# Performance work log

Measured on AMD Instinct MI355X. Metric: run time of the kernel, lower is better.

## Reference

```python
import jax, jax.numpy as jnp
import numpy as np

EPS = 1e-6
CHUNK = 64
GATE_LOGIT_NORMALIZER = 16.0
NUM_HEADS = 4


def _rms(x, w):
    return x * jax.lax.rsqrt(jnp.mean(x * x, axis=-1, keepdims=True) + EPS) * w


def _gla_chunk(q, k, v, glog, num_heads):
    # q,k: [B,T,Dk] v: [B,T,Dv] glog: [B,T,Dk] (log decay, <=0)
    B, T, Dk = q.shape
    Dv = v.shape[-1]
    dk, dv = Dk // num_heads, Dv // num_heads
    Nc = T // CHUNK

    def split(x, d):
        # [B,T,H*d] -> [B,H,Nc,C,d]
        return x.reshape(B, T, num_heads, d).transpose(0, 2, 1, 3).reshape(B, num_heads, Nc, CHUNK, d)

    q, k, v, g = split(q, dk), split(k, dk), split(v, dv), split(glog, dk)
    b = jnp.cumsum(g, axis=3)  # inclusive cumulative log-decay within chunk
    scale = dk ** -0.5
    qe = q * jnp.exp(b) * scale

    # intra-chunk: A[t,s] = sum_d q_t k_s exp(b_t - b_s), causal (t>=s)
    mask = jnp.tril(jnp.ones((CHUNK, CHUNK), dtype=bool))
    A = jnp.einsum('bhncd,bhnsd->bhncs', qe, k * jnp.exp(-b))
    A = jnp.where(mask, A, 0.0)
    o_intra = jnp.einsum('bhncs,bhnsd->bhncd', A, v)

    # inter-chunk recurrence over state S: [B,H,dk,dv]
    def step(S, xs):
        qe_c, k_c, v_c, b_c = xs  # [B,H,C,*]
        blast = b_c[:, :, -1, :]                      # [B,H,dk]
        o_inter = jnp.einsum('bhcd,bhde->bhce', qe_c, S)
        kd = k_c * jnp.exp(blast[:, :, None, :] - b_c)
        S_new = S * jnp.exp(blast)[..., None] + jnp.einsum('bhcd,bhce->bhde', kd, v_c)
        return S_new, o_inter

    S0 = jnp.zeros((B, num_heads, dk, dv), q.dtype)
    xs = tuple(jnp.moveaxis(t, 2, 0) for t in (qe, k, v, b))
    _, o_inter = jax.lax.scan(step, S0, xs)
    o = o_intra + jnp.moveaxis(o_inter, 0, 2)  # [B,H,Nc,C,dv]
    return o.reshape(B, num_heads, T, dv).transpose(0, 2, 1, 3)  # [B,T,H,dv]


def setup_inputs() -> dict:
    key = jax.random.key(0)
    ks = jax.random.split(key, 12)
    B, T, Hs = 4, 2048, 1024
    Dk, Dv, I, R = 512, 1024, 2816, 16
    p = lambda k, s: jax.random.normal(k, s, jnp.float32) * 0.02
    return {
        'hidden_states': jax.random.normal(ks[0], (B, T, Hs), jnp.float32),
        'attn_norm_w': jnp.ones((Hs,), jnp.float32),
        'Wq': p(ks[1], (Hs, Dk)), 'Wk': p(ks[2], (Hs, Dk)), 'Wv': p(ks[3], (Hs, Dv)),
        'Wg': p(ks[4], (Hs, Dv)),
        'Wgk1': p(ks[5], (Hs, R)), 'Wgk2': p(ks[6], (R, Dk)), 'bgk2': jnp.zeros((Dk,), jnp.float32),
        'gnorm_w': jnp.ones((Dv // NUM_HEADS,), jnp.float32),
        'Wo': p(ks[7], (Dv, Hs)),
        'mlp_norm_w': jnp.ones((Hs,), jnp.float32),
        'W_gate': p(ks[8], (Hs, I)), 'W_up': p(ks[9], (Hs, I)), 'W_down': p(ks[10], (I, Hs)),
    }


def reference(hidden_states, attn_norm_w, Wq, Wk, Wv, Wg, Wgk1, Wgk2, bgk2,
              gnorm_w, Wo, mlp_norm_w, W_gate, W_up, W_down):
    x = hidden_states
    h = _rms(x, attn_norm_w)
    q, k, v = h @ Wq, h @ Wk, h @ Wv
    glog = jax.nn.log_sigmoid(h @ Wgk1 @ Wgk2 + bgk2) / GATE_LOGIT_NORMALIZER
    o = _gla_chunk(q, k, v, glog, NUM_HEADS)          # [B,T,H,dv]
    g_out = (h @ Wg).reshape(o.shape)
    o = _rms(o, gnorm_w) * (g_out * jax.nn.sigmoid(g_out))  # per-head RMSNorm + swish gate
    attn_out = o.reshape(x.shape[0], x.shape[1], -1) @ Wo
    # fused residual RMSNorm
    x2 = attn_out + x
    n = _rms(x2, mlp_norm_w)
    mlp = (jax.nn.silu(n @ W_gate) * (n @ W_up)) @ W_down
    return x2 + mlp
```

## Files before the change

kernel.cpp:

```cpp
#include <hip/hip_runtime.h>

typedef unsigned short u16;
typedef __attribute__((ext_vector_type(8))) short bf8_t;
typedef __attribute__((ext_vector_type(4))) float f4_t;

#define MFMA_B16(a,b,c) __builtin_amdgcn_mfma_f32_16x16x32_bf16(a,b,c,0,0,0)

#define TOKS 8192
#define HS   1024
#define DKTOT 512
#define DVTOT 1024
#define IM   2816

constexpr size_t OFF_WQT    = 0;
constexpr size_t OFF_WKT    = OFF_WQT    + (size_t)DKTOT*HS*2;
constexpr size_t OFF_WVT    = OFF_WKT    + (size_t)DKTOT*HS*2;
constexpr size_t OFF_WGT    = OFF_WVT    + (size_t)DVTOT*HS*2;
constexpr size_t OFF_WOT    = OFF_WGT    + (size_t)DVTOT*HS*2;
constexpr size_t OFF_WGATET = OFF_WOT    + (size_t)HS*DVTOT*2;
constexpr size_t OFF_WUPT   = OFF_WGATET + (size_t)IM*HS*2;
constexpr size_t OFF_WDOWNT = OFF_WUPT   + (size_t)IM*HS*2;
constexpr size_t OFF_QE     = OFF_WDOWNT + (size_t)HS*IM*2;
constexpr size_t OFF_CTST   = OFF_QE     + (size_t)TOKS*DKTOT*2;
constexpr size_t OFF_DEC    = OFF_CTST   + (size_t)512*256*128*2;
constexpr size_t OFF_R1     = OFF_DEC    + (size_t)512*128*4;
constexpr size_t OFF_QKB    = OFF_R1;
constexpr size_t OFF_GLOG   = OFF_QKB    + (size_t)TOKS*1024*2;
constexpr size_t OFF_VT     = OFF_GLOG   + (size_t)TOKS*DKTOT*4;
constexpr size_t OFF_UP     = OFF_R1;
constexpr size_t OFF_R3     = OFF_R1 + 50331648;
constexpr size_t OFF_H      = OFF_R3;
constexpr size_t OFF_OI     = OFF_R3;
constexpr size_t OFF_N2     = OFF_R3;
constexpr size_t OFF_R4     = OFF_R3 + 16777216;
constexpr size_t OFF_GO     = OFF_R4;
constexpr size_t OFF_OG     = OFF_R4;
constexpr size_t WS_NEED    = OFF_R4 + 16777216;

__device__ __forceinline__ u16 f2bf(float f){
  union{ float f; unsigned u; } x; x.f = f;
  unsigned r = x.u + 0x7FFFu + ((x.u >> 16) & 1u);
  return (u16)(r >> 16);
}
__device__ __forceinline__ float bf2f(u16 u){
  union{ unsigned u; float f; } x; x.u = ((unsigned)u) << 16; return x.f;
}
__device__ __forceinline__ void gl_lds16(const void* g, void* l){
  __builtin_amdgcn_global_load_lds(
      (const __attribute__((address_space(1))) unsigned int*)g,
      (__attribute__((address_space(3))) unsigned int*)l, 16, 0, 0);
}
__device__ __forceinline__ int swz128(int row, int cb){ return row*128 + (cb ^ ((row & 7)  << 4)); }
__device__ __forceinline__ int swz256(int row, int cb){ return row*256 + (cb ^ ((row & 15) << 4)); }

__device__ __forceinline__ void xcd_map(int gx, int gy, int& bm, int& bn){
  const int i   = blockIdx.y*gx + blockIdx.x;
  const int cpx = (gx*gy) >> 3;
  const int j   = (i & 7)*cpx + (i >> 3);
  const int k   = j / (gx*8);
  const int jl  = j - k*(gx*8);
  bn = jl >> 3;
  bm = k*8 + (jl & 7);
}

struct TransAll {
  const float* src[8];
  u16* dst[8];
  int K[8];
  int N[8];
  int end[8];
};

__global__ __launch_bounds__(256) void k_transpose_all(TransAll ta)
{
  __shared__ float tile[64][65];
  const int flat = blockIdx.x;
  int seg = 0, start = 0;
  #pragma unroll
  for(int j=0;j<8;j++){
    if(flat >= ta.end[j]){ seg = j+1; start = ta.end[j]; }
  }
  const float* W = ta.src[seg];
  u16* Wt = ta.dst[seg];
  const int K = ta.K[seg], N = ta.N[seg];
  const int local = flat - start;
  const int tilesX = N >> 6;
  const int n0 = (local % tilesX)*64, k0 = (local / tilesX)*64;
  const int tx = threadIdx.x & 63, tg = threadIdx.x >> 6;
  #pragma unroll
  for(int i=0;i<16;i++){
    int kr = tg*16 + i;
    tile[kr][tx] = W[(size_t)(k0+kr)*N + n0 + tx];
  }
  __syncthreads();
  #pragma unroll
  for(int i=0;i<16;i++){
    int nr = tg*16 + i;
    Wt[(size_t)(n0+nr)*K + k0 + tx] = f2bf(tile[tx][nr]);
  }
}

__global__ __launch_bounds__(256) void k_rmsnorm(
    const float* __restrict__ X, const float* __restrict__ W, u16* __restrict__ H)
{
  __shared__ float red[4];
  const size_t row = blockIdx.x;
  const int t = threadIdx.x;
  const float4 v = ((const float4*)(X + row*1024))[t];
  float ss = v.x*v.x + v.y*v.y + v.z*v.z + v.w*v.w;
  #pragma unroll
  for(int m=32;m>=1;m>>=1) ss += __shfl_xor(ss, m, 64);
  if((t & 63) == 0) red[t >> 6] = ss;
  __syncthreads();
  ss = red[0] + red[1] + red[2] + red[3];
  const float rs = rsqrtf(ss*(1.f/1024.f) + 1e-6f);
  const float4 w = ((const float4*)W)[t];
  ushort4 o;
  o.x = f2bf(v.x*rs*w.x);
  o.y = f2bf(v.y*rs*w.y);
  o.z = f2bf(v.z*rs*w.z);
  o.w = f2bf(v.w*rs*w.w);
  ((ushort4*)H)[row*256 + t] = o;
}

__global__ __launch_bounds__(256) void k_glog(
    const u16* __restrict__ H, const float* __restrict__ W1,
    const float* __restrict__ W2, const float* __restrict__ bias,
    float* __restrict__ G)
{
  __shared__ float hs[1024];
  __shared__ float red[16][17];
  __shared__ float rr[16];
  const size_t row = blockIdx.x;
  const int t = threadIdx.x;
  #pragma unroll
  for(int j=0;j<4;j++) hs[t*4+j] = bf2f(H[row*1024 + t*4 + j]);
  __syncthreads();
  const int r = t & 15, c = t >> 4;
  float acc = 0.f;
  #pragma unroll
  for(int j=0;j<64;j++){
    int k = c*64 + ((j + c) & 63);
    acc += hs[k] * W1[(size_t)k*16 + r];
  }
  red[c][r] = acc;
  __syncthreads();
  if(t < 16){
    float s2 = 0.f;
    #pragma unroll
    for(int cc=0;cc<16;cc++) s2 += red[cc][t];
    rr[t] = s2;
  }
  __syncthreads();
  #pragma unroll
  for(int dd=0;dd<2;dd++){
    int dcol = t + dd*256;
    float z = bias[dcol];
    #pragma unroll
    for(int j=0;j<16;j++) z += rr[j]*W2[j*512 + dcol];
    float ls = fminf(z, 0.f) - log1pf(__expf(-fabsf(z)));
    G[row*512 + dcol] = ls * 0.0625f;
  }
}

enum { E_BF16=1, E_ADDF32=2, E_SILUMUL=3, E_TRANS=4, E_QKVG=5 };

template<int EPI>
__global__ __launch_bounds__(512, 2) void k_gemm8(
    const u16* __restrict__ A, const u16* __restrict__ Bt,
    void* __restrict__ Cp, const void* __restrict__ aux,
    int M, int N, int K)
{
  __shared__ __align__(16) u16 lds[3*24576];
  const int t = threadIdx.x;
  const int wv = t >> 6, ln = t & 63, lr = ln & 15, lg = ln >> 4;
  const int wm = wv >> 2, wn = wv & 3;
  int bm, bn; xcd_map(gridDim.x, gridDim.y, bm, bn);
  const int m0 = bm*128, n0 = bn*256;
  const int NT = K >> 6;

  const int sr = t >> 3;
  const int sc = ((t & 7)*16 ^ ((sr & 7) << 4)) >> 1;
  const u16* Asrc = A  + (size_t)(m0 + sr)*K + sc;
  const u16* Bsrc = Bt + (size_t)(n0 + sr)*K + sc;

  auto stage = [&](int T){
    const int b = T % 3;
    const size_t ko = (size_t)T * 64;
    u16* dA = lds + b*24576 + wv*512;
    u16* dB = lds + b*24576 + 8192 + wv*512;
    gl_lds16(Asrc + ko,                    dA);
    gl_lds16(Asrc + (size_t)64*K + ko,     dA + 4096);
    #pragma unroll
    for(int j=0;j<4;j++)
      gl_lds16(Bsrc + (size_t)(j*64)*K + ko, dB + j*4096);
  };

  f4_t acc[4][4];
  #pragma unroll
  for(int i=0;i<4;i++)
    #pragma unroll
    for(int j=0;j<4;j++) acc[i][j] = f4_t{0.f,0.f,0.f,0.f};

  const int rA = wm*64 + lr;
  const int rB = wn*64 + lr;
  const int cxor = (lr & 7) << 4;

  auto compute = [&](int b){
    const char* La = (const char*)(lds + b*24576);
    const char* Lb = La + 16384;
    #pragma unroll
    for(int kk=0;kk<2;++kk){
      const int cb = (kk*64 + lg*16) ^ cxor;
      bf8_t af[4], bfr[4];
      #pragma unroll
      for(int m=0;m<4;m++) af[m]  = *(const bf8_t*)(La + (rA + m*16)*128 + cb);
      #pragma unroll
      for(int n=0;n<4;n++) bfr[n] = *(const bf8_t*)(Lb + (rB + n*16)*128 + cb);
      __builtin_amdgcn_s_setprio(1);
      #pragma unroll
      for(int m=0;m<4;m++)
        #pragma unroll
        for(int n=0;n<4;n++)
          acc[m][n] = MFMA_B16(af[m], bfr[n], acc[m][n]);
      __builtin_amdgcn_s_setprio(0);
    }
  };

  stage(0);
  stage(1);

  for(int T=0; T<NT-1; ++T){
    asm volatile("s_waitcnt vmcnt(6)" ::: "memory");
    __builtin_amdgcn_s_barrier();
    asm volatile("" ::: "memory");
    __builtin_amdgcn_sched_barrier(0);
    if(T+2 < NT) stage(T+2);
    compute(T % 3);
  }
  asm volatile("s_waitcnt vmcnt(0)" ::: "memory");
  __builtin_amdgcn_s_barrier();
  asm volatile("" ::: "memory");
  __builtin_amdgcn_sched_barrier(0);
  compute((NT-1) % 3);

  #pragma unroll
  for(int m=0;m<4;m++){
    #pragma unroll
    for(int n=0;n<4;n++){
      const int row0 = m0 + wm*64 + m*16 + lg*4;
      const int col  = n0 + wn*64 + n*16 + lr;
      if constexpr(EPI==E_TRANS){
        ushort4 u;
        u.x = f2bf(acc[m][n][0]); u.y = f2bf(acc[m][n][1]);
        u.z = f2bf(acc[m][n][2]); u.w = f2bf(acc[m][n][3]);
        *(ushort4*)((u16*)Cp + (size_t)col*M + row0) = u;
      } else if constexpr(EPI==E_QKVG){
        char* wsb = (char*)Cp;
        if(n0 < 1024){
          u16* dst = (u16*)(wsb + OFF_QKB);
          #pragma unroll
          for(int r=0;r<4;r++) dst[(size_t)(row0+r)*1024 + col] = f2bf(acc[m][n][r]);
        } else if(n0 < 2048){
          u16* dst = (u16*)(wsb + OFF_VT);
          ushort4 u;
          u.x = f2bf(acc[m][n][0]); u.y = f2bf(acc[m][n][1]);
          u.z = f2bf(acc[m][n][2]); u.w = f2bf(acc[m][n][3]);
          *(ushort4*)(dst + (size_t)(col-1024)*TOKS + row0) = u;
        } else {
          u16* dst = (u16*)(wsb + OFF_GO);
          #pragma unroll
          for(int r=0;r<4;r++) dst[(size_t)(row0+r)*1024 + (col-2048)] = f2bf(acc[m][n][r]);
        }
      } else {
        #pragma unroll
        for(int r=0;r<4;r++){
          const size_t idx = (size_t)(row0+r)*N + col;
          float v = acc[m][n][r];
          if constexpr(EPI==E_BF16) ((u16*)Cp)[idx] = f2bf(v);
          else if constexpr(EPI==E_ADDF32) ((float*)Cp)[idx] = v + ((const float*)aux)[idx];
          else if constexpr(EPI==E_SILUMUL){
            float u = bf2f(((const u16*)aux)[idx]);
            ((u16*)Cp)[idx] = f2bf(u * v / (1.f + __expf(-v)));
          }
        }
      }
    }
  }
}

__global__ __launch_bounds__(256) void k_gla_a(
    const u16* __restrict__ QK,
    const u16* __restrict__ VT, const float* __restrict__ G,
    u16* __restrict__ QE, u16* __restrict__ OI,
    u16* __restrict__ CT, float* __restrict__ DEC)
{
  __shared__ __align__(16) u16 qe_s[64*128];
  __shared__ __align__(16) u16 ke_s[64*128];
  __shared__ __align__(16) u16 kd_s[128*64];
  __shared__ __align__(16) u16 a_s [64*64];
  __shared__ float ps_s[2][128];

  const int bid = blockIdx.x;
  const int nc = bid & 31, hh = (bid >> 5) & 3, bb = bid >> 7;
  const int bh = bb*4 + hh;
  const int tok0 = bb*2048 + nc*64;
  const int t = threadIdx.x;
  const size_t cbase = (size_t)(bh*32 + nc);

  {
    const int d = t & 127;
    const int half = t >> 7;
    const int col = hh*128 + d;
    const int i0 = half*32;
    float g[32];
    float psum = 0.f;
    #pragma unroll
    for(int i=0;i<32;i++){
      g[i] = G[(size_t)(tok0+i0+i)*512 + col];
      psum += g[i];
    }
    ps_s[half][d] = psum;
    __syncthreads();
    const float cum0  = half ? ps_s[0][d] : 0.f;
    const float blast = ps_s[0][d] + ps_s[1][d];
    if(half == 0) DEC[cbase*128 + d] = __expf(blast);
    float cum = cum0;
    #pragma unroll
    for(int i=0;i<32;i++){
      cum += g[i];
      const int tok = tok0 + i0 + i;
      float qv = bf2f(QK[(size_t)tok*1024 + col]);
      float kv = bf2f(QK[(size_t)tok*1024 + 512 + col]);
      float qe = qv * __expf(cum) * 0.08838834764831845f;
      float ke = kv * __expf(-cum);
      float kd = kv * __expf(blast - cum);
      *(u16*)((char*)qe_s + swz256(i0+i, d*2)) = f2bf(qe);
      *(u16*)((char*)ke_s + swz256(i0+i, d*2)) = f2bf(ke);
      *(u16*)((char*)kd_s + swz128(d, (i0+i)*2)) = f2bf(kd);
      QE[(cbase*64 + i0+i)*128 + d] = f2bf(qe);
    }
  }
  __syncthreads();

  const int wv = t >> 6, ln = t & 63, lr = ln & 15, lg = ln >> 4;

  bf8_t aq[4];
  #pragma unroll
  for(int ks=0;ks<4;ks++)
    aq[ks] = *(const bf8_t*)((const char*)qe_s + swz256(wv*16 + lr, ks*64 + lg*16));
  #pragma unroll
  for(int n=0;n<4;n++){
    f4_t accA = f4_t{0.f,0.f,0.f,0.f};
    #pragma unroll
    for(int ks=0;ks<4;ks++){
      bf8_t bk = *(const bf8_t*)((const char*)ke_s + swz256(n*16 + lr, ks*64 + lg*16));
      accA = MFMA_B16(aq[ks], bk, accA);
    }
    #pragma unroll
    for(int r=0;r<4;r++){
      int i = wv*16 + lg*4 + r;
      int s = n*16 + lr;
      float v = (s <= i) ? accA[r] : 0.f;
      *(u16*)((char*)a_s + swz128(i, s*2)) = f2bf(v);
    }
  }
  __syncthreads();

  bf8_t af[2], kf[2][2];
  #pragma unroll
  for(int ks=0;ks<2;ks++)
    af[ks] = *(const bf8_t*)((const char*)a_s + swz128(wv*16 + lr, ks*64 + lg*16));
  #pragma unroll
  for(int p=0;p<2;p++)
    #pragma unroll
    for(int ks=0;ks<2;ks++)
      kf[p][ks] = *(const bf8_t*)((const char*)kd_s + swz128((2*wv+p)*16 + lr, ks*64 + lg*16));

  #pragma unroll 4
  for(int ne=0; ne<16; ne++){
    bf8_t vf[2];
    #pragma unroll
    for(int ks=0;ks<2;ks++)
      vf[ks] = *(const bf8_t*)(VT + (size_t)(hh*256 + ne*16 + lr)*8192 + tok0 + ks*32 + lg*8);
    f4_t ao = f4_t{0.f,0.f,0.f,0.f};
    ao = MFMA_B16(af[0], vf[0], ao);
    ao = MFMA_B16(af[1], vf[1], ao);
    #pragma unroll
    for(int r=0;r<4;r++)
      OI[(cbase*64 + wv*16 + lg*4 + r)*256 + ne*16 + lr] = f2bf(ao[r]);
    f4_t c0 = f4_t{0.f,0.f,0.f,0.f}, c1 = f4_t{0.f,0.f,0.f,0.f};
    c0 = MFMA_B16(kf[0][0], vf[0], c0);
    c0 = MFMA_B16(kf[0][1], vf[1], c0);
    c1 = MFMA_B16(kf[1][0], vf[0], c1);
    c1 = MFMA_B16(kf[1][1], vf[1], c1);
    u16* dst = CT + (cbase*256 + ne*16 + lr)*128;
    ushort4 u0, u1;
    u0.x=f2bf(c0[0]); u0.y=f2bf(c0[1]); u0.z=f2bf(c0[2]); u0.w=f2bf(c0[3]);
    u1.x=f2bf(c1[0]); u1.y=f2bf(c1[1]); u1.z=f2bf(c1[2]); u1.w=f2bf(c1[3]);
    *(ushort4*)(dst + (2*wv+0)*16 + lg*4) = u0;
    *(ushort4*)(dst + (2*wv+1)*16 + lg*4) = u1;
  }
}

__global__ __launch_bounds__(256) void k_scan(
    u16* __restrict__ CTST, const float* __restrict__ DEC)
{
  const int idx = blockIdx.x*256 + threadIdx.x;
  const int d = idx & 127;
  const int e = (idx >> 7) & 255;
  const int bh = idx >> 15;
  float s = 0.f;
  for(int n=0;n<32;n++){
    const size_t off = ((size_t)(bh*32 + n)*256 + e)*128 + d;
    float c = bf2f(CTST[off]);
    CTST[off] = f2bf(s);
    s = s * DEC[(bh*32+n)*128 + d] + c;
  }
}

__global__ __launch_bounds__(256) void k_gla_c(
    const u16* __restrict__ QE, const u16* __restrict__ ST,
    const u16* __restrict__ OI, const u16* __restrict__ GO,
    const float* __restrict__ GW, u16* __restrict__ OG)
{
  const int bid = blockIdx.x;
  const int nc = bid & 31, hh = (bid >> 5) & 3, bb = bid >> 7;
  const int bh = bb*4 + hh;
  const int tok0 = bb*2048 + nc*64;
  const int t = threadIdx.x;
  const int wv = t >> 6, ln = t & 63, lr = ln & 15, lg = ln >> 4;
  const size_t cbase = (size_t)(bh*32 + nc);

  bf8_t qf[4];
  #pragma unroll
  for(int ks=0;ks<4;ks++)
    qf[ks] = *(const bf8_t*)(QE + (cbase*64 + wv*16 + lr)*128 + ks*32 + lg*8);

  f4_t acc[16];
  #pragma unroll
  for(int ne=0;ne<16;ne++){
    f4_t a = f4_t{0.f,0.f,0.f,0.f};
    #pragma unroll
    for(int ks=0;ks<4;ks++){
      bf8_t sf = *(const bf8_t*)(ST + (cbase*256 + ne*16 + lr)*128 + ks*32 + lg*8);
      a = MFMA_B16(qf[ks], sf, a);
    }
    acc[ne] = a;
  }

  float vals[16][4];
  float ss[4] = {0.f,0.f,0.f,0.f};
  #pragma unroll
  for(int ne=0;ne<16;ne++)
    #pragma unroll
    for(int r=0;r<4;r++){
      float v = acc[ne][r] + bf2f(OI[(cbase*64 + wv*16 + lg*4 + r)*256 + ne*16 + lr]);
      vals[ne][r] = v;
      ss[r] += v*v;
    }
  #pragma unroll
  for(int r=0;r<4;r++){
    ss[r] += __shfl_xor(ss[r], 1, 64);
    ss[r] += __shfl_xor(ss[r], 2, 64);
    ss[r] += __shfl_xor(ss[r], 4, 64);
    ss[r] += __shfl_xor(ss[r], 8, 64);
  }
  float rs[4];
  #pragma unroll
  for(int r=0;r<4;r++) rs[r] = rsqrtf(ss[r]*(1.f/256.f) + 1e-6f);

  #pragma unroll
  for(int ne=0;ne<16;ne++)
    #pragma unroll
    for(int r=0;r<4;r++){
      int i = wv*16 + lg*4 + r;
      int e = ne*16 + lr;
      const size_t idx = (size_t)(tok0+i)*1024 + hh*256 + e;
      float gg = bf2f(GO[idx]);
      float sg = gg / (1.f + __expf(-gg));
      OG[idx] = f2bf(vals[ne][r]*rs[r]*GW[e]*sg);
    }
}

extern "C" void kernel_launch(void* const* d_in, const int* in_sizes, int n_in,
                              void* d_out, int out_size, void* d_ws, size_t ws_size,
                              hipStream_t stream) {
  (void)in_sizes; (void)n_in; (void)out_size;
  if (ws_size < WS_NEED) return;

  const float* x       = (const float*)d_in[0];
  const float* attn_w  = (const float*)d_in[1];
  const float* Wq      = (const float*)d_in[2];
  const float* Wk      = (const float*)d_in[3];
  const float* Wv      = (const float*)d_in[4];
  const float* Wg      = (const float*)d_in[5];
  const float* Wgk1    = (const float*)d_in[6];
  const float* Wgk2    = (const float*)d_in[7];
  const float* bgk2    = (const float*)d_in[8];
  const float* gnw     = (const float*)d_in[9];
  const float* Wo      = (const float*)d_in[10];
  const float* mlpw    = (const float*)d_in[11];
  const float* Wgate   = (const float*)d_in[12];
  const float* Wup     = (const float*)d_in[13];
  const float* Wdown   = (const float*)d_in[14];
  char* ws = (char*)d_ws;

  u16*   wqt   = (u16*)(ws + OFF_WQT);
  u16*   wkt   = (u16*)(ws + OFF_WKT);
  u16*   wvt   = (u16*)(ws + OFF_WVT);
  u16*   wgt   = (u16*)(ws + OFF_WGT);
  u16*   wot   = (u16*)(ws + OFF_WOT);
  u16*   wgatet= (u16*)(ws + OFF_WGATET);
  u16*   wupt  = (u16*)(ws + OFF_WUPT);
  u16*   wdownt= (u16*)(ws + OFF_WDOWNT);
  u16*   qeb   = (u16*)(ws + OFF_QE);
  u16*   ctst  = (u16*)(ws + OFF_CTST);
  float* decb  = (float*)(ws + OFF_DEC);
  u16*   qkb   = (u16*)(ws + OFF_QKB);
  float* glogb = (float*)(ws + OFF_GLOG);
  u16*   vtb   = (u16*)(ws + OFF_VT);
  u16*   upb   = (u16*)(ws + OFF_UP);
  u16*   hb    = (u16*)(ws + OFF_H);
  u16*   oib   = (u16*)(ws + OFF_OI);
  u16*   n2b   = (u16*)(ws + OFF_N2);
  u16*   gob   = (u16*)(ws + OFF_GO);
  u16*   ogb   = (u16*)(ws + OFF_OG);
  float* x2b   = (float*)d_out;

  dim3 blk(256);
  dim3 blk8(512);

  TransAll ta;
  ta.src[0]=Wq;    ta.dst[0]=wqt;    ta.K[0]=HS;  ta.N[0]=DKTOT;
  ta.src[1]=Wk;    ta.dst[1]=wkt;    ta.K[1]=HS;  ta.N[1]=DKTOT;
  ta.src[2]=Wv;    ta.dst[2]=wvt;    ta.K[2]=HS;  ta.N[2]=DVTOT;
  ta.src[3]=Wg;    ta.dst[3]=wgt;    ta.K[3]=HS;  ta.N[3]=DVTOT;
  ta.src[4]=Wo;    ta.dst[4]=wot;    ta.K[4]=DVTOT; ta.N[4]=HS;
  ta.src[5]=Wgate; ta.dst[5]=wgatet; ta.K[5]=HS;  ta.N[5]=IM;
  ta.src[6]=Wup;   ta.dst[6]=wupt;   ta.K[6]=HS;  ta.N[6]=IM;
  ta.src[7]=Wdown; ta.dst[7]=wdownt; ta.K[7]=IM;  ta.N[7]=HS;
  {
    int cum = 0;
    for(int j=0;j<8;j++){ cum += (ta.N[j]>>6)*(ta.K[j]>>6); ta.end[j] = cum; }
  }
  k_transpose_all<<<3136, blk, 0, stream>>>(ta);

  k_rmsnorm<<<TOKS, blk, 0, stream>>>(x, attn_w, hb);
  k_gemm8<E_QKVG><<<dim3(12, 64), blk8, 0, stream>>>(hb, wqt, ws, nullptr, TOKS, 3072, HS);
  k_glog<<<TOKS, blk, 0, stream>>>(hb, Wgk1, Wgk2, bgk2, glogb);

  k_gla_a<<<512, blk, 0, stream>>>(qkb, vtb, glogb, qeb, oib, ctst, decb);
  k_scan <<<2048, blk, 0, stream>>>(ctst, decb);
  k_gla_c<<<512, blk, 0, stream>>>(qeb, ctst, oib, gob, gnw, ogb);

  k_gemm8<E_ADDF32><<<dim3(4, 64), blk8, 0, stream>>>(ogb, wot, x2b, x, TOKS, HS, DVTOT);

  k_rmsnorm<<<TOKS, blk, 0, stream>>>(x2b, mlpw, n2b);
  k_gemm8<E_BF16>   <<<dim3(11, 64), blk8, 0, stream>>>(n2b, wupt,   upb, nullptr, TOKS, IM, HS);
  k_gemm8<E_SILUMUL><<<dim3(11, 64), blk8, 0, stream>>>(n2b, wgatet, upb, upb,     TOKS, IM, HS);
  k_gemm8<E_ADDF32> <<<dim3(4, 64),  blk8, 0, stream>>>(upb, wdownt, x2b, x2b,     TOKS, HS, IM);
}
```

Baseline: 418.4 us.

## Reshape GEMM tile to 256x128 with double-buffered LDS and split-phase barriers

The bf16 GEMM kernel's block tile changes from 128x256 to 256x128, with the 8 waves rearranged into a 4x2 grid, and all launch grids are recomputed to match. The three-stage LDS ring is replaced by two buffers. The next K-tile's global-to-LDS copy is issued after the first half-step's fragment reads, and each iteration waits for all outstanding loads before swapping buffers. This is meant to cut LDS footprint and restructure load/compute overlap, but a shallower prefetch depth and two barriers per half-step may expose more memory latency. The unused transposing epilogue is removed.

```diff
diff --git a/kernel.cpp b/kernel.cpp
--- a/kernel.cpp
+++ b/kernel.cpp
@@ -163,20 +163,20 @@
   }
 }
 
-enum { E_BF16=1, E_ADDF32=2, E_SILUMUL=3, E_TRANS=4, E_QKVG=5 };
+enum { E_BF16=1, E_ADDF32=2, E_SILUMUL=3, E_QKVG=5 };
 
 template<int EPI>
-__global__ __launch_bounds__(512, 2) void k_gemm8(
+__global__ __launch_bounds__(512, 2) void k_gemm9(
     const u16* __restrict__ A, const u16* __restrict__ Bt,
     void* __restrict__ Cp, const void* __restrict__ aux,
     int M, int N, int K)
 {
-  __shared__ __align__(16) u16 lds[3*24576];
+  __shared__ __align__(16) u16 lds[49152];
   const int t = threadIdx.x;
   const int wv = t >> 6, ln = t & 63, lr = ln & 15, lg = ln >> 4;
-  const int wm = wv >> 2, wn = wv & 3;
+  const int wm = wv >> 1, wn = wv & 1;
   int bm, bn; xcd_map(gridDim.x, gridDim.y, bm, bn);
-  const int m0 = bm*128, n0 = bn*256;
+  const int m0 = bm*256, n0 = bn*128;
   const int NT = K >> 6;
 
   const int sr = t >> 3;
@@ -184,16 +184,17 @@
   const u16* Asrc = A  + (size_t)(m0 + sr)*K + sc;
   const u16* Bsrc = Bt + (size_t)(n0 + sr)*K + sc;
 
-  auto stage = [&](int T){
-    const int b = T % 3;
-    const size_t ko = (size_t)T * 64;
-    u16* dA = lds + b*24576 + wv*512;
-    u16* dB = lds + b*24576 + 8192 + wv*512;
+  auto stage_full = [&](int Tn){
+    const int pb = (Tn & 1) * 24576;
+    const size_t ko = (size_t)Tn * 64;
+    u16* dA = lds + pb + wv*512;
+    u16* dB = lds + pb + 16384 + wv*512;
     gl_lds16(Asrc + ko,                    dA);
-    gl_lds16(Asrc + (size_t)64*K + ko,     dA + 4096);
-    #pragma unroll
-    for(int j=0;j<4;j++)
-      gl_lds16(Bsrc + (size_t)(j*64)*K + ko, dB + j*4096);
+    gl_lds16(Asrc + (size_t)64*K  + ko,    dA + 4096);
+    gl_lds16(Asrc + (size_t)128*K + ko,    dA + 8192);
+    gl_lds16(Asrc + (size_t)192*K + ko,    dA + 12288);
+    gl_lds16(Bsrc + ko,                    dB);
+    gl_lds16(Bsrc + (size_t)64*K  + ko,    dB + 4096);
   };
 
   f4_t acc[4][4];
@@ -202,47 +203,42 @@
     #pragma unroll
     for(int j=0;j<4;j++) acc[i][j] = f4_t{0.f,0.f,0.f,0.f};
 
-  const int rA = wm*64 + lr;
-  const int rB = wn*64 + lr;
   const int cxor = (lr & 7) << 4;
 
-  auto compute = [&](int b){
-    const char* La = (const char*)(lds + b*24576);
-    const char* Lb = La + 16384;
-    #pragma unroll
-    for(int kk=0;kk<2;++kk){
-      const int cb = (kk*64 + lg*16) ^ cxor;
-      bf8_t af[4], bfr[4];
+  stage_full(0);
+  asm volatile("s_waitcnt vmcnt(0)" ::: "memory");
+  __builtin_amdgcn_s_barrier();
+  asm volatile("" ::: "memory");
+
+  for(int T=0; T<NT; ++T){
+    const char* Lc = (const char*)lds + (T & 1)*49152;
+    const bool more = (T+1 < NT);
+    #pragma unroll
+    for(int p=0;p<2;++p){
+      const int cb = (p*64 + lg*16) ^ cxor;
+      bf8_t af[4], bfv[4];
       #pragma unroll
-      for(int m=0;m<4;m++) af[m]  = *(const bf8_t*)(La + (rA + m*16)*128 + cb);
+      for(int m=0;m<4;m++) af[m]  = *(const bf8_t*)(Lc + (wm*64 + m*16 + lr)*128 + cb);
       #pragma unroll
-      for(int n=0;n<4;n++) bfr[n] = *(const bf8_t*)(Lb + (rB + n*16)*128 + cb);
+      for(int n=0;n<4;n++) bfv[n] = *(const bf8_t*)(Lc + 32768 + (wn*64 + n*16 + lr)*128 + cb);
+      if(p == 0 && more) stage_full(T+1);
+      asm volatile("" ::: "memory");
+      __builtin_amdgcn_s_barrier();
+      asm volatile("s_waitcnt lgkmcnt(0)" ::: "memory");
+      __builtin_amdgcn_sched_barrier(0);
       __builtin_amdgcn_s_setprio(1);
       #pragma unroll
       for(int m=0;m<4;m++)
         #pragma unroll
         for(int n=0;n<4;n++)
-          acc[m][n] = MFMA_B16(af[m], bfr[n], acc[m][n]);
+          acc[m][n] = MFMA_B16(af[m], bfv[n], acc[m][n]);
       __builtin_amdgcn_s_setprio(0);
-    }
-  };
-
-  stage(0);
-  stage(1);
-
-  for(int T=0; T<NT-1; ++T){
-    asm volatile("s_waitcnt vmcnt(6)" ::: "memory");
-    __builtin_amdgcn_s_barrier();
-    asm volatile("" ::: "memory");
-    __builtin_amdgcn_sched_barrier(0);
-    if(T+2 < NT) stage(T+2);
-    compute(T % 3);
-  }
-  asm volatile("s_waitcnt vmcnt(0)" ::: "memory");
-  __builtin_amdgcn_s_barrier();
-  asm volatile("" ::: "memory");
-  __builtin_amdgcn_sched_barrier(0);
-  compute((NT-1) % 3);
+      if(p == 1 && more) asm volatile("s_waitcnt vmcnt(0)" ::: "memory");
+      asm volatile("" ::: "memory");
+      __builtin_amdgcn_s_barrier();
+      asm volatile("" ::: "memory");
+    }
+  }
 
   #pragma unroll
   for(int m=0;m<4;m++){
@@ -250,12 +246,7 @@
     for(int n=0;n<4;n++){
       const int row0 = m0 + wm*64 + m*16 + lg*4;
       const int col  = n0 + wn*64 + n*16 + lr;
-      if constexpr(EPI==E_TRANS){
-        ushort4 u;
-        u.x = f2bf(acc[m][n][0]); u.y = f2bf(acc[m][n][1]);
-        u.z = f2bf(acc[m][n][2]); u.w = f2bf(acc[m][n][3]);
-        *(ushort4*)((u16*)Cp + (size_t)col*M + row0) = u;
-      } else if constexpr(EPI==E_QKVG){
+      if constexpr(EPI==E_QKVG){
         char* wsb = (char*)Cp;
         if(n0 < 1024){
           u16* dst = (u16*)(wsb + OFF_QKB);
@@ -529,7 +520,7 @@
   float* x2b   = (float*)d_out;
 
   dim3 blk(256);
-  dim3 blk8(512);
+  dim3 blk9(512);
 
   TransAll ta;
   ta.src[0]=Wq;    ta.dst[0]=wqt;    ta.K[0]=HS;  ta.N[0]=DKTOT;
@@ -547,17 +538,17 @@
   k_transpose_all<<<3136, blk, 0, stream>>>(ta);
 
   k_rmsnorm<<<TOKS, blk, 0, stream>>>(x, attn_w, hb);
-  k_gemm8<E_QKVG><<<dim3(12, 64), blk8, 0, stream>>>(hb, wqt, ws, nullptr, TOKS, 3072, HS);
+  k_gemm9<E_QKVG><<<dim3(24, 32), blk9, 0, stream>>>(hb, wqt, ws, nullptr, TOKS, 3072, HS);
   k_glog<<<TOKS, blk, 0, stream>>>(hb, Wgk1, Wgk2, bgk2, glogb);
 
   k_gla_a<<<512, blk, 0, stream>>>(qkb, vtb, glogb, qeb, oib, ctst, decb);
   k_scan <<<2048, blk, 0, stream>>>(ctst, decb);
   k_gla_c<<<512, blk, 0, stream>>>(qeb, ctst, oib, gob, gnw, ogb);
 
-  k_gemm8<E_ADDF32><<<dim3(4, 64), blk8, 0, stream>>>(ogb, wot, x2b, x, TOKS, HS, DVTOT);
+  k_gemm9<E_ADDF32><<<dim3(8, 32), blk9, 0, stream>>>(ogb, wot, x2b, x, TOKS, HS, DVTOT);
 
   k_rmsnorm<<<TOKS, blk, 0, stream>>>(x2b, mlpw, n2b);
-  k_gemm8<E_BF16>   <<<dim3(11, 64), blk8, 0, stream>>>(n2b, wupt,   upb, nullptr, TOKS, IM, HS);
-  k_gemm8<E_SILUMUL><<<dim3(11, 64), blk8, 0, stream>>>(n2b, wgatet, upb, upb,     TOKS, IM, HS);
-  k_gemm8<E_ADDF32> <<<dim3(4, 64),  blk8, 0, stream>>>(upb, wdownt, x2b, x2b,     TOKS, HS, IM);
-}
+  k_gemm9<E_BF16>   <<<dim3(22, 32), blk9, 0, stream>>>(n2b, wupt,   upb, nullptr, TOKS, IM, HS);
+  k_gemm9<E_SILUMUL><<<dim3(22, 32), blk9, 0, stream>>>(n2b, wgatet, upb, upb,     TOKS, IM, HS);
+  k_gemm9<E_ADDF32> <<<dim3(8, 32),  blk9, 0, stream>>>(upb, wdownt, x2b, x2b,     TOKS, HS, IM);
+}
```

Measured after the change: 443.7 us. 1.06x slower.
